# Optimization experiments

Hardware: AMD Instinct MI355X
Metric: run time of the kernel (lower is better)

The kernel has to match this reference:

```python
import jax, jax.numpy as jnp
import numpy as np

N = 100000
E = 1600000
NFEAT = 256
NHIDDEN = 128
NCLASS = 40
NLAYERS = 8
INIT_T = 0.5


def setup_inputs() -> dict:
    key = jax.random.key(0)
    ks = jax.random.split(key, 9)
    x = jax.random.normal(ks[0], (N, NFEAT), dtype=jnp.float32)
    edge_row = jax.random.randint(ks[1], (E,), 0, N, dtype=jnp.int32)
    edge_col = jax.random.randint(ks[2], (E,), 0, N, dtype=jnp.int32)
    # small weights so the Chebyshev recurrence stays numerically tame
    edge_weight = jax.random.uniform(ks[3], (E,), dtype=jnp.float32) * (2.0 / 16.0)
    b1 = 1.0 / np.sqrt(NFEAT)
    fc1_w = jax.random.uniform(ks[4], (NFEAT, NHIDDEN), minval=-b1, maxval=b1, dtype=jnp.float32)
    fc1_b = jax.random.uniform(ks[5], (NHIDDEN,), minval=-b1, maxval=b1, dtype=jnp.float32)
    b2 = 1.0 / np.sqrt(NHIDDEN)
    fc2_w = jax.random.uniform(ks[6], (NHIDDEN, NCLASS), minval=-b2, maxval=b2, dtype=jnp.float32)
    fc2_b = jax.random.uniform(ks[7], (NCLASS,), minval=-b2, maxval=b2, dtype=jnp.float32)
    thetas = jnp.full((NLAYERS,), INIT_T, dtype=jnp.float32)
    return {"x": x, "edge_row": edge_row, "edge_col": edge_col,
            "edge_weight": edge_weight, "fc1_w": fc1_w, "fc1_b": fc1_b,
            "fc2_w": fc2_w, "fc2_b": fc2_b, "thetas": thetas}


def _spmm(edge_row, edge_col, edge_weight, t):
    # out[r] = sum_{e: row[e]=r} w[e] * t[col[e]]   (sparse L @ T)
    msgs = edge_weight[:, None] * t[edge_col]  # [E, H]
    return jax.ops.segment_sum(msgs, edge_row, num_segments=N)


def reference(x, edge_row, edge_col, edge_weight, fc1_w, fc1_b, fc2_w, fc2_b, thetas):
    # eval mode: dropout is identity
    h = jax.nn.relu(x @ fc1_w + fc1_b)  # [N, H]
    # filter 0: T_0 = h, poly = theta_0 * T_0
    t0 = h
    poly = thetas[0] * t0
    # filter 1: T_1 = L @ T_0
    t1 = _spmm(edge_row, edge_col, edge_weight, t0)
    poly = poly + thetas[1] * t1
    # remaining filters, replicating the original prevs-update order exactly
    prev0, prev1 = t0, t1
    for i in range(2, NLAYERS):
        ti = 2.0 * _spmm(edge_row, edge_col, edge_weight, prev0) - prev1
        prev1 = prev0
        prev0 = ti
        poly = poly + thetas[i] * ti
    y = poly @ fc2_w + fc2_b  # [N, nclass]
    return jax.nn.log_softmax(y, axis=1)
```

## Files before the change

kernel.cpp:

```cpp
#include <hip/hip_runtime.h>
#include <hip/hip_bf16.h>


#define NFEAT 256
#define NHID  128
#define NCLS  40
#define ELLS  48
#define NXCD  8

typedef __hip_bfloat16 bf16;
typedef __attribute__((ext_vector_type(8))) short bf16x8;
typedef __attribute__((ext_vector_type(4))) float f32x4;

__device__ inline float2 load2b(const bf16* p) {
    __hip_bfloat162 v = *(const __hip_bfloat162*)p;
    return make_float2(__bfloat162float(v.x), __bfloat162float(v.y));
}
__device__ inline void store2b(bf16* p, float2 v) {
    __hip_bfloat162 o;
    o.x = __float2bfloat16(v.x);
    o.y = __float2bfloat16(v.y);
    *(__hip_bfloat162*)p = o;
}

__global__ void zero_ints(int* __restrict__ p, int n) {
    int i = blockIdx.x * blockDim.x + threadIdx.x;
    if (i < n) p[i] = 0;
}

__global__ __launch_bounds__(256) void scatter_ell_xcd(
    const int* __restrict__ erow, const int* __restrict__ ecol,
    const float* __restrict__ ew, int* __restrict__ deg,
    int2* __restrict__ cw, int E, int n, int nslices) {
    const int b = blockIdx.x;
    const int g = b & (NXCD - 1);
    const int s = b >> 3;
    const int rlo = (int)(((long long)n * g) / NXCD);
    const int rhi = (int)(((long long)n * (g + 1)) / NXCD);
    const int per = (E + nslices - 1) / nslices;
    const int e0 = s * per;
    const int e1 = (e0 + per < E) ? e0 + per : E;
    for (int e = e0 + (int)threadIdx.x; e < e1; e += 256) {
        int r = erow[e];
        if (r >= rlo && r < rhi) {
            int c = ecol[e];
            float w = ew[e];
            int p = atomicAdd(&deg[r], 1);
            if (p < ELLS)
                cw[(size_t)r * ELLS + p] = make_int2(c, __float_as_int(w));
        }
    }
}

__global__ void hist_kernel(const int* __restrict__ erow, int* __restrict__ deg, int E) {
    int e = blockIdx.x * blockDim.x + threadIdx.x;
    if (e < E) atomicAdd(&deg[erow[e]], 1);
}

__global__ void assign_starts(const int* __restrict__ deg, int* __restrict__ counter,
                              int* __restrict__ row_start, int* __restrict__ cursor, int N) {
    int r = blockIdx.x * blockDim.x + threadIdx.x;
    int lane = threadIdx.x & 63;
    int d = (r < N) ? deg[r] : 0;
    int x = d;
    #pragma unroll
    for (int off = 1; off < 64; off <<= 1) {
        int y = __shfl_up(x, off);
        if (lane >= off) x += y;
    }
    int base = 0;
    if (lane == 63) base = atomicAdd(counter, x);
    base = __shfl(base, 63);
    int start = base + (x - d);
    if (r < N) {
        row_start[r] = start;
        cursor[r] = start;
    }
}

__global__ void scatter_compact(const int* __restrict__ erow, const int* __restrict__ ecol,
                                const float* __restrict__ ew, int* __restrict__ cursor,
                                int2* __restrict__ cw, int E) {
    int e = blockIdx.x * blockDim.x + threadIdx.x;
    if (e < E) {
        int r = erow[e];
        int p = atomicAdd(&cursor[r], 1);
        cw[p] = make_int2(ecol[e], __float_as_int(ew[e]));
    }
}

__global__ __launch_bounds__(256) void fc1_mfma(
    const float* __restrict__ x, const float* __restrict__ W,
    const float* __restrict__ bias, bf16* __restrict__ t0, int n) {
    __shared__ __align__(16) bf16 As[128 * 40];
    __shared__ __align__(16) bf16 Bs[128 * 40];

    const int tid = threadIdx.x;
    const int wave = tid >> 6;
    const int lane = tid & 63;
    const int quad = lane >> 4;
    const int lm = lane & 15;
    const int block_row = blockIdx.x * 128;

    f32x4 acc[2][8];
    #pragma unroll
    for (int s = 0; s < 2; ++s)
        #pragma unroll
        for (int t = 0; t < 8; ++t)
            acc[s][t] = (f32x4){0.f, 0.f, 0.f, 0.f};

    float bcol[8];
    #pragma unroll
    for (int t = 0; t < 8; ++t) bcol[t] = bias[t * 16 + lm];

    for (int kc = 0; kc < NFEAT; kc += 32) {
        #pragma unroll
        for (int i = 0; i < 4; ++i) {
            int idx = tid + 256 * i;
            int row = idx >> 3;
            int c4 = idx & 7;
            int grow = block_row + row;
            float4 v = make_float4(0.f, 0.f, 0.f, 0.f);
            if (grow < n) v = *(const float4*)&x[(size_t)grow * NFEAT + kc + c4 * 4];
            __hip_bfloat162 lo2, hi2;
            lo2.x = __float2bfloat16(v.x); lo2.y = __float2bfloat16(v.y);
            hi2.x = __float2bfloat16(v.z); hi2.y = __float2bfloat16(v.w);
            *(__hip_bfloat162*)&As[row * 40 + c4 * 4] = lo2;
            *(__hip_bfloat162*)&As[row * 40 + c4 * 4 + 2] = hi2;
        }
        #pragma unroll
        for (int i = 0; i < 4; ++i) {
            int idx = tid + 256 * i;
            int nn = idx & 127;
            int k4 = idx >> 7;
            const float* wp = &W[(size_t)(kc + k4 * 4) * NHID + nn];
            float v0 = wp[0];
            float v1 = wp[NHID];
            float v2 = wp[2 * NHID];
            float v3 = wp[3 * NHID];
            __hip_bfloat162 lo2, hi2;
            lo2.x = __float2bfloat16(v0); lo2.y = __float2bfloat16(v1);
            hi2.x = __float2bfloat16(v2); hi2.y = __float2bfloat16(v3);
            *(__hip_bfloat162*)&Bs[nn * 40 + k4 * 4] = lo2;
            *(__hip_bfloat162*)&Bs[nn * 40 + k4 * 4 + 2] = hi2;
        }
        __syncthreads();

        bf16x8 af0 = *(const bf16x8*)&As[(wave * 32 + lm) * 40 + quad * 8];
        bf16x8 af1 = *(const bf16x8*)&As[(wave * 32 + 16 + lm) * 40 + quad * 8];
        #pragma unroll
        for (int t = 0; t < 8; ++t) {
            bf16x8 bf = *(const bf16x8*)&Bs[(t * 16 + lm) * 40 + quad * 8];
            acc[0][t] = __builtin_amdgcn_mfma_f32_16x16x32_bf16(af0, bf, acc[0][t], 0, 0, 0);
            acc[1][t] = __builtin_amdgcn_mfma_f32_16x16x32_bf16(af1, bf, acc[1][t], 0, 0, 0);
        }
        __syncthreads();
    }

    #pragma unroll
    for (int s = 0; s < 2; ++s) {
        #pragma unroll
        for (int r = 0; r < 4; ++r) {
            int grow = block_row + wave * 32 + s * 16 + quad * 4 + r;
            if (grow >= n) continue;
            bf16* orow = t0 + (size_t)grow * NHID + lm;
            #pragma unroll
            for (int t = 0; t < 8; ++t) {
                float v = fmaxf(acc[s][t][r] + bcol[t], 0.f);
                orow[t * 16] = __float2bfloat16(v);
            }
        }
    }
}

template <bool FIRST, int PMODE>
__global__ __launch_bounds__(256) void spmm_cheb(
    const int* __restrict__ row_start, const int* __restrict__ deg,
    const int2* __restrict__ cw,
    const bf16* __restrict__ tprev, const bf16* __restrict__ tsub,
    bf16* __restrict__ tout, float* __restrict__ poly,
    const float* __restrict__ thetas, int layer, int ell_stride, int n) {
    int lane = threadIdx.x & 63;
    int wid = (int)((blockIdx.x * (unsigned)blockDim.x + threadIdx.x) >> 6);
    if (wid >= n) return;
    int start = ell_stride ? wid * ell_stride : row_start[wid];
    int d = deg[wid];
    const int2* ep = cw + start;
    const int lo = 2 * lane;

    float2 acc = make_float2(0.f, 0.f);
    int j = 0;
    for (; j + 8 <= d; j += 8) {
        int2 e[8];
        #pragma unroll
        for (int u = 0; u < 8; ++u) e[u] = ep[j + u];
        float2 tv[8];
        #pragma unroll
        for (int u = 0; u < 8; ++u) tv[u] = load2b(tprev + (size_t)e[u].x * NHID + lo);
        #pragma unroll
        for (int u = 0; u < 8; ++u) {
            float w = __int_as_float(e[u].y);
            acc.x = fmaf(w, tv[u].x, acc.x);
            acc.y = fmaf(w, tv[u].y, acc.y);
        }
    }
    for (; j < d; ++j) {
        int2 e = ep[j];
        float w = __int_as_float(e.y);
        float2 tv = load2b(tprev + (size_t)e.x * NHID + lo);
        acc.x = fmaf(w, tv.x, acc.x);
        acc.y = fmaf(w, tv.y, acc.y);
    }

    size_t o = (size_t)wid * NHID + lo;
    float2 res, pv;
    if constexpr (FIRST) {
        res = acc;
    } else {
        pv = load2b(tsub + o);
        res = make_float2(2.f * acc.x - pv.x, 2.f * acc.y - pv.y);
    }
    store2b(tout + o, res);

    if constexpr (PMODE == 1) {
        float th0 = thetas[0], th1 = thetas[1], th2 = thetas[2];
        float2 t0v = load2b(tprev + o);
        float2 p;
        p.x = th0 * t0v.x + th1 * pv.x + th2 * res.x;
        p.y = th0 * t0v.y + th1 * pv.y + th2 * res.y;
        *(float2*)&poly[o] = p;
    } else if constexpr (PMODE == 2) {
        float tha = thetas[layer - 1], thb = thetas[layer];
        float2 tp = load2b(tprev + o);
        float2 p = *(float2*)&poly[o];
        p.x += tha * tp.x + thb * res.x;
        p.y += tha * tp.y + thb * res.y;
        *(float2*)&poly[o] = p;
    } else if constexpr (PMODE == 3) {
        float thb = thetas[layer];
        float2 p = *(float2*)&poly[o];
        p.x += thb * res.x;
        p.y += thb * res.y;
        *(float2*)&poly[o] = p;
    }
}

__global__ __launch_bounds__(256) void fc2_softmax(
    const float* __restrict__ poly, const float* __restrict__ w2,
    const float* __restrict__ b2, float* __restrict__ out, int n) {
    int row = blockIdx.x * 256 + threadIdx.x;
    if (row >= n) return;

    float acc[NCLS];
    #pragma unroll
    for (int c = 0; c < NCLS; ++c) acc[c] = b2[c];

    const float* pr = poly + (size_t)row * NHID;
    #pragma unroll 1
    for (int k = 0; k < NHID; k += 4) {
        float4 p = *(const float4*)&pr[k];
        const float* wr = w2 + (size_t)k * NCLS;
        #pragma unroll
        for (int c = 0; c < NCLS; ++c) {
            acc[c] = fmaf(p.x, wr[c], acc[c]);
            acc[c] = fmaf(p.y, wr[NCLS + c], acc[c]);
            acc[c] = fmaf(p.z, wr[2 * NCLS + c], acc[c]);
            acc[c] = fmaf(p.w, wr[3 * NCLS + c], acc[c]);
        }
    }

    float m = acc[0];
    #pragma unroll
    for (int c = 1; c < NCLS; ++c) m = fmaxf(m, acc[c]);
    float s = 0.f;
    #pragma unroll
    for (int c = 0; c < NCLS; ++c) s += __expf(acc[c] - m);
    float lse = m + __logf(s);

    float* orow = out + (size_t)row * NCLS;
    #pragma unroll
    for (int c = 0; c < NCLS; c += 4) {
        float4 v = make_float4(acc[c] - lse, acc[c + 1] - lse,
                               acc[c + 2] - lse, acc[c + 3] - lse);
        *(float4*)&orow[c] = v;
    }
}

static void run_pipeline(const float* x, const float* w1, const float* b1,
                         const float* w2, const float* b2, const float* thetas,
                         float* out, int N, int E,
                         const int* row_start, const int* deg, const int2* cw,
                         int ell_stride, float* poly, bf16* tX, bf16* tY, bf16* tZ,
                         hipStream_t stream) {
    fc1_mfma<<<(N + 127) / 128, 256, 0, stream>>>(x, w1, b1, tX, N);

    int spmm_blocks = (int)(((size_t)N * 64 + 255) / 256);
    spmm_cheb<true, 0><<<spmm_blocks, 256, 0, stream>>>(
        row_start, deg, cw, tX, (const bf16*)nullptr, tY, poly, thetas, 1, ell_stride, N);
    bf16* p0 = tX;
    bf16* p1 = tY;
    bf16* dead = tZ;
    for (int i = 2; i < 8; ++i) {
        if (i == 2)       spmm_cheb<false, 1><<<spmm_blocks, 256, 0, stream>>>(
            row_start, deg, cw, p0, p1, dead, poly, thetas, i, ell_stride, N);
        else if (i == 4 || i == 6) spmm_cheb<false, 2><<<spmm_blocks, 256, 0, stream>>>(
            row_start, deg, cw, p0, p1, dead, poly, thetas, i, ell_stride, N);
        else if (i == 7)  spmm_cheb<false, 3><<<spmm_blocks, 256, 0, stream>>>(
            row_start, deg, cw, p0, p1, dead, poly, thetas, i, ell_stride, N);
        else              spmm_cheb<false, 0><<<spmm_blocks, 256, 0, stream>>>(
            row_start, deg, cw, p0, p1, dead, poly, thetas, i, ell_stride, N);
        bf16* nd = p1;
        p1 = p0;
        p0 = dead;
        dead = nd;
    }
    fc2_softmax<<<(N + 255) / 256, 256, 0, stream>>>(poly, w2, b2, out, N);
}

extern "C" void kernel_launch(void* const* d_in, const int* in_sizes, int n_in,
                              void* d_out, int out_size, void* d_ws, size_t ws_size,
                              hipStream_t stream) {
    const float* x      = (const float*)d_in[0];
    const int*   erow   = (const int*)d_in[1];
    const int*   ecol   = (const int*)d_in[2];
    const float* ew     = (const float*)d_in[3];
    const float* w1     = (const float*)d_in[4];
    const float* b1     = (const float*)d_in[5];
    const float* w2     = (const float*)d_in[6];
    const float* b2     = (const float*)d_in[7];
    const float* thetas = (const float*)d_in[8];
    float* out = (float*)d_out;

    const int N = in_sizes[0] / NFEAT;
    const int E = in_sizes[1];

    size_t need_ell = 4096 + (size_t)N * 4 + (size_t)N * ELLS * 8 +
                      (size_t)N * NHID * 4 + 3 * (size_t)N * NHID * 2 + 4096;
    bool use_ell = need_ell <= ws_size;

    char* ws = (char*)d_ws;
    size_t off = 0;
    auto alloc = [&](size_t bytes) -> void* {
        off = (off + 255) & ~(size_t)255;
        void* p = ws + off;
        off += bytes;
        return p;
    };

    if (use_ell) {
        int*   deg  = (int*)alloc((size_t)N * 4);
        int2*  cw   = (int2*)alloc((size_t)N * ELLS * 8);
        float* poly = (float*)alloc((size_t)N * NHID * 4);
        bf16*  tX   = (bf16*)alloc((size_t)N * NHID * 2);
        bf16*  tY   = (bf16*)alloc((size_t)N * NHID * 2);
        bf16*  tZ   = (bf16*)alloc((size_t)N * NHID * 2);

        zero_ints<<<(N + 255) / 256, 256, 0, stream>>>(deg, N);
        const int nslices = 128;
        scatter_ell_xcd<<<nslices * NXCD, 256, 0, stream>>>(erow, ecol, ew, deg, cw, E, N, nslices);
        run_pipeline(x, w1, b1, w2, b2, thetas, out, N, E,
                     nullptr, deg, cw, ELLS, poly, tX, tY, tZ, stream);
    } else {
        int*   deg       = (int*)alloc((size_t)(N + 1) * 4);
        int*   counter   = deg + N;
        int*   row_start = (int*)alloc((size_t)N * 4);
        int*   cursor    = (int*)alloc((size_t)N * 4);
        int2*  cw        = (int2*)alloc((size_t)E * 8);
        float* poly      = (float*)alloc((size_t)N * NHID * 4);
        bf16*  tX        = (bf16*)alloc((size_t)N * NHID * 2);
        bf16*  tY        = (bf16*)alloc((size_t)N * NHID * 2);
        bf16*  tZ        = (bf16*)alloc((size_t)N * NHID * 2);

        zero_ints<<<(N + 1 + 255) / 256, 256, 0, stream>>>(deg, N + 1);
        hist_kernel<<<(E + 255) / 256, 256, 0, stream>>>(erow, deg, E);
        assign_starts<<<(N + 255) / 256, 256, 0, stream>>>(deg, counter, row_start, cursor, N);
        scatter_compact<<<(E + 255) / 256, 256, 0, stream>>>(erow, ecol, ew, cursor, cw, E);
        run_pipeline(x, w1, b1, w2, b2, thetas, out, N, E,
                     row_start, deg, cw, 0, poly, tX, tY, tZ, stream);
    }
}
```

Before: 931.0 us.

## Chunk feature dimension into 16-wide column slabs for cache-local SpMM gathers

Stores hidden features (T buffers and poly) in a chunked layout of 8 slabs of 16 columns each. Each SpMM block now handles one slab for 32 rows, so with blockIdx&7 selecting the slab, blocks on the same XCD gather from a smaller 3.2MB slab that can stay resident in L2. Each gather is 32 bytes per row instead of 256, which cuts contiguous bytes per access but improves cache hit rate. It also skips the unused T store in the last layer, and adapts fc1 output and fc2 input indexing.

After: 1.200 ms. 1.29x slower.

```diff
diff --git a/kernel.cpp b/kernel.cpp
--- a/kernel.cpp
+++ b/kernel.cpp
@@ -4,6 +4,8 @@
 
 #define NFEAT 256
 #define NHID  128
+#define NCHUNK 8
+#define CHW   16
 #define NCLS  40
 #define ELLS  48
 #define NXCD  8
@@ -163,11 +165,10 @@
         for (int r = 0; r < 4; ++r) {
             int grow = block_row + wave * 32 + s * 16 + quad * 4 + r;
             if (grow >= n) continue;
-            bf16* orow = t0 + (size_t)grow * NHID + lm;
             #pragma unroll
             for (int t = 0; t < 8; ++t) {
                 float v = fmaxf(acc[s][t][r] + bcol[t], 0.f);
-                orow[t * 16] = __float2bfloat16(v);
+                t0[((size_t)t * n + grow) * CHW + lm] = __float2bfloat16(v);
             }
         }
     }
@@ -180,13 +181,19 @@
     const bf16* __restrict__ tprev, const bf16* __restrict__ tsub,
     bf16* __restrict__ tout, float* __restrict__ poly,
     const float* __restrict__ thetas, int layer, int ell_stride, int n) {
-    int lane = threadIdx.x & 63;
-    int wid = (int)((blockIdx.x * (unsigned)blockDim.x + threadIdx.x) >> 6);
-    if (wid >= n) return;
-    int start = ell_stride ? wid * ell_stride : row_start[wid];
-    int d = deg[wid];
+    const int fc = blockIdx.x & 7;
+    const int slice = blockIdx.x >> 3;
+    const int lane = threadIdx.x & 63;
+    const int wave = threadIdx.x >> 6;
+    const int grp = lane >> 3;
+    const int fl = (lane & 7) * 2;
+    const int r = slice * 32 + wave * 8 + grp;
+    if (r >= n) return;
+
+    int start = ell_stride ? r * ell_stride : row_start[r];
+    int d = deg[r];
     const int2* ep = cw + start;
-    const int lo = 2 * lane;
+    const bf16* tp = tprev + (size_t)fc * n * CHW;
 
     float2 acc = make_float2(0.f, 0.f);
     int j = 0;
@@ -196,7 +203,7 @@
         for (int u = 0; u < 8; ++u) e[u] = ep[j + u];
         float2 tv[8];
         #pragma unroll
-        for (int u = 0; u < 8; ++u) tv[u] = load2b(tprev + (size_t)e[u].x * NHID + lo);
+        for (int u = 0; u < 8; ++u) tv[u] = load2b(tp + (size_t)e[u].x * CHW + fl);
         #pragma unroll
         for (int u = 0; u < 8; ++u) {
             float w = __int_as_float(e[u].y);
@@ -207,12 +214,12 @@
     for (; j < d; ++j) {
         int2 e = ep[j];
         float w = __int_as_float(e.y);
-        float2 tv = load2b(tprev + (size_t)e.x * NHID + lo);
+        float2 tv = load2b(tp + (size_t)e.x * CHW + fl);
         acc.x = fmaf(w, tv.x, acc.x);
         acc.y = fmaf(w, tv.y, acc.y);
     }
 
-    size_t o = (size_t)wid * NHID + lo;
+    size_t o = ((size_t)fc * n + r) * CHW + fl;
     float2 res, pv;
     if constexpr (FIRST) {
         res = acc;
@@ -220,7 +227,7 @@
         pv = load2b(tsub + o);
         res = make_float2(2.f * acc.x - pv.x, 2.f * acc.y - pv.y);
     }
-    store2b(tout + o, res);
+    if constexpr (PMODE != 3) store2b(tout + o, res);
 
     if constexpr (PMODE == 1) {
         float th0 = thetas[0], th1 = thetas[1], th2 = thetas[2];
@@ -231,10 +238,10 @@
         *(float2*)&poly[o] = p;
     } else if constexpr (PMODE == 2) {
         float tha = thetas[layer - 1], thb = thetas[layer];
-        float2 tp = load2b(tprev + o);
+        float2 tp2 = load2b(tprev + o);
         float2 p = *(float2*)&poly[o];
-        p.x += tha * tp.x + thb * res.x;
-        p.y += tha * tp.y + thb * res.y;
+        p.x += tha * tp2.x + thb * res.x;
+        p.y += tha * tp2.y + thb * res.y;
         *(float2*)&poly[o] = p;
     } else if constexpr (PMODE == 3) {
         float thb = thetas[layer];
@@ -255,17 +262,20 @@
     #pragma unroll
     for (int c = 0; c < NCLS; ++c) acc[c] = b2[c];
 
-    const float* pr = poly + (size_t)row * NHID;
     #pragma unroll 1
-    for (int k = 0; k < NHID; k += 4) {
-        float4 p = *(const float4*)&pr[k];
-        const float* wr = w2 + (size_t)k * NCLS;
-        #pragma unroll
-        for (int c = 0; c < NCLS; ++c) {
-            acc[c] = fmaf(p.x, wr[c], acc[c]);
-            acc[c] = fmaf(p.y, wr[NCLS + c], acc[c]);
-            acc[c] = fmaf(p.z, wr[2 * NCLS + c], acc[c]);
-            acc[c] = fmaf(p.w, wr[3 * NCLS + c], acc[c]);
+    for (int fc = 0; fc < NCHUNK; ++fc) {
+        const float* pc = poly + ((size_t)fc * n + row) * CHW;
+        #pragma unroll
+        for (int k4 = 0; k4 < 4; ++k4) {
+            float4 p = *(const float4*)&pc[k4 * 4];
+            const float* wr = w2 + (size_t)(fc * CHW + k4 * 4) * NCLS;
+            #pragma unroll
+            for (int c = 0; c < NCLS; ++c) {
+                acc[c] = fmaf(p.x, wr[c], acc[c]);
+                acc[c] = fmaf(p.y, wr[NCLS + c], acc[c]);
+                acc[c] = fmaf(p.z, wr[2 * NCLS + c], acc[c]);
+                acc[c] = fmaf(p.w, wr[3 * NCLS + c], acc[c]);
+            }
         }
     }
 
@@ -294,7 +304,7 @@
                          hipStream_t stream) {
     fc1_mfma<<<(N + 127) / 128, 256, 0, stream>>>(x, w1, b1, tX, N);
 
-    int spmm_blocks = (int)(((size_t)N * 64 + 255) / 256);
+    int spmm_blocks = ((N + 31) / 32) * NCHUNK;
     spmm_cheb<true, 0><<<spmm_blocks, 256, 0, stream>>>(
         row_start, deg, cw, tX, (const bf16*)nullptr, tY, poly, thetas, 1, ell_stride, N);
     bf16* p0 = tX;
```
